# Optimization experiments

Measured on AMD Instinct MI355X. Metric: run time of the kernel, lower is better.

The kernel has to match this reference:

```python
import jax, jax.numpy as jnp
import numpy as np

N_NODES = 50000
IN_DIM = 128
N_EDGES = 500000


def setup_inputs() -> dict:
    key = jax.random.key(0)
    k1, k2, k3, k4 = jax.random.split(key, 4)
    x = jax.random.normal(k1, (N_NODES, IN_DIM), dtype=jnp.float32)
    edge_index = jax.random.randint(k2, (2, N_EDGES), 0, N_NODES, dtype=jnp.int64)
    edge_weight = jax.random.uniform(k3, (N_EDGES,), dtype=jnp.float32)
    # Linear(2*in_dim -> 1): weight flattened to [2*in_dim], scalar bias
    W = jax.random.normal(k4, (2 * IN_DIM,), dtype=jnp.float32) * (1.0 / np.sqrt(2 * IN_DIM))
    b = jnp.zeros((1,), dtype=jnp.float32)
    return {"x": x, "edge_index": edge_index, "edge_weight": edge_weight, "W": W, "b": b}


def reference(x, edge_index, edge_weight, W, b):
    src, dst = edge_index[0], edge_index[1]
    d = x.shape[-1]
    # cat([x[src], x[dst]]) @ W == x[src] @ W[:d] + x[dst] @ W[d:]
    # Pre-project nodes once ([N] each) instead of materializing [E, 2d]
    proj_src = x @ W[:d]          # [N]
    proj_dst = x @ W[d:]          # [N]
    logits = proj_src[src] + proj_dst[dst] + b[0]   # [E]
    prompt_scores = jax.nn.sigmoid(logits)
    return edge_weight * prompt_scores
```

## Files before the change

### kernel.cpp

```cpp
#include <hip/hip_runtime.h>
#include <hip/hip_bf16.h>


#define IN_DIM 128
#define BLOCK 256

__global__ void __launch_bounds__(BLOCK)
edgeprompt_proj(const float* __restrict__ x,
                const float* __restrict__ W,
                float* __restrict__ proj,
                int n_nodes) {
    const int lane = threadIdx.x & 63;
    const int half = lane >> 5;
    const int sl   = lane & 31;
    const int wave = (blockIdx.x * blockDim.x + threadIdx.x) >> 6;

    const float4 ws = *reinterpret_cast<const float4*>(&W[sl * 4]);
    const float4 wd = *reinterpret_cast<const float4*>(&W[IN_DIM + sl * 4]);

    const int n = wave * 2 + half;
    if (n >= n_nodes) return;

    const float4 xv = *reinterpret_cast<const float4*>(&x[(size_t)n * IN_DIM + sl * 4]);
    float ps = xv.x * ws.x + xv.y * ws.y + xv.z * ws.z + xv.w * ws.w;
    float pd = xv.x * wd.x + xv.y * wd.y + xv.z * wd.z + xv.w * wd.w;
    #pragma unroll
    for (int off = 16; off > 0; off >>= 1) {
        ps += __shfl_xor(ps, off);
        pd += __shfl_xor(pd, off);
    }
    if (sl == 0) {
        proj[n] = ps;
        proj[n_nodes + n] = pd;
    }
}

__global__ void __launch_bounds__(BLOCK)
edgeprompt_edges(const int* __restrict__ edge_index,
                 const float* __restrict__ edge_weight,
                 const float* __restrict__ proj,
                 const float* __restrict__ bias_p,
                 float* __restrict__ out,
                 int n_edges, int n_nodes) {
    const int tid = blockIdx.x * blockDim.x + threadIdx.x;
    const float bias = bias_p[0];
    const float* __restrict__ proj_d = proj + n_nodes;

    const int q = tid;
    const int nquads = n_edges >> 2;
    if (q < nquads) {
        const int4   s4 = *reinterpret_cast<const int4*>(&edge_index[q * 4]);
        const int4   d4 = *reinterpret_cast<const int4*>(&edge_index[n_edges + q * 4]);
        const float4 w4 = *reinterpret_cast<const float4*>(&edge_weight[q * 4]);
        float4 o;
        o.x = w4.x / (1.0f + __expf(-(proj[s4.x] + proj_d[d4.x] + bias)));
        o.y = w4.y / (1.0f + __expf(-(proj[s4.y] + proj_d[d4.y] + bias)));
        o.z = w4.z / (1.0f + __expf(-(proj[s4.z] + proj_d[d4.z] + bias)));
        o.w = w4.w / (1.0f + __expf(-(proj[s4.w] + proj_d[d4.w] + bias)));
        *reinterpret_cast<float4*>(&out[q * 4]) = o;
    }
    const int e = (nquads << 2) + tid;
    if (e < n_edges) {
        const int s = edge_index[e];
        const int d = edge_index[n_edges + e];
        out[e] = edge_weight[e] / (1.0f + __expf(-(proj[s] + proj_d[d] + bias)));
    }
}

extern "C" void kernel_launch(void* const* d_in, const int* in_sizes, int n_in,
                              void* d_out, int out_size, void* d_ws, size_t ws_size,
                              hipStream_t stream) {
    const float* x           = (const float*)d_in[0];
    const int*   edge_index  = (const int*)d_in[1];
    const float* edge_weight = (const float*)d_in[2];
    const float* W           = (const float*)d_in[3];
    const float* b           = (const float*)d_in[4];
    float* out = (float*)d_out;

    const int n_nodes = in_sizes[0] / IN_DIM;
    const int n_edges = in_sizes[2];
    float* proj = (float*)d_ws;

    const int blocks1 = (n_nodes + 7) / 8;
    edgeprompt_proj<<<blocks1, BLOCK, 0, stream>>>(x, W, proj, n_nodes);

    const int blocks2 = ((n_edges + 3) / 4 + BLOCK - 1) / BLOCK;
    edgeprompt_edges<<<blocks2, BLOCK, 0, stream>>>(edge_index, edge_weight, proj, b,
                                                    out, n_edges, n_nodes);
}
```

Measured before the change: 17.26 us.

## Grid-stride node projection with 4 nodes per wave; nontemporal edge loads/stores

The projection kernel now assigns four nodes per wave, using 16 lanes per node with two float4 loads each. It runs a grid-stride loop over a capped grid of 2048 blocks instead of launching one block per 8 nodes. The edge kernel switches its streaming index, weight and output accesses to nontemporal loads and stores so they do not pollute cache, keeping the gathered proj array resident. The trade-off is fewer waves in flight for the projection and more per-lane work; nontemporal hints can also slow things if the hardware handles them poorly.

```diff
diff --git a/kernel.cpp b/kernel.cpp
--- a/kernel.cpp
+++ b/kernel.cpp
@@ -4,6 +4,10 @@
 
 #define IN_DIM 128
 #define BLOCK 256
+#define K1_BLOCKS 2048
+
+typedef int   i32x4 __attribute__((ext_vector_type(4)));
+typedef float f32x4 __attribute__((ext_vector_type(4)));
 
 __global__ void __launch_bounds__(BLOCK)
 edgeprompt_proj(const float* __restrict__ x,
@@ -11,27 +15,38 @@
                 float* __restrict__ proj,
                 int n_nodes) {
     const int lane = threadIdx.x & 63;
-    const int half = lane >> 5;
-    const int sl   = lane & 31;
+    const int g    = lane >> 4;
+    const int sg   = lane & 15;
     const int wave = (blockIdx.x * blockDim.x + threadIdx.x) >> 6;
+    const int nwaves = (gridDim.x * blockDim.x) >> 6;
 
-    const float4 ws = *reinterpret_cast<const float4*>(&W[sl * 4]);
-    const float4 wd = *reinterpret_cast<const float4*>(&W[IN_DIM + sl * 4]);
+    const f32x4 ws0 = *reinterpret_cast<const f32x4*>(&W[sg * 4]);
+    const f32x4 ws1 = *reinterpret_cast<const f32x4*>(&W[64 + sg * 4]);
+    const f32x4 wd0 = *reinterpret_cast<const f32x4*>(&W[IN_DIM + sg * 4]);
+    const f32x4 wd1 = *reinterpret_cast<const f32x4*>(&W[IN_DIM + 64 + sg * 4]);
 
-    const int n = wave * 2 + half;
-    if (n >= n_nodes) return;
-
-    const float4 xv = *reinterpret_cast<const float4*>(&x[(size_t)n * IN_DIM + sl * 4]);
-    float ps = xv.x * ws.x + xv.y * ws.y + xv.z * ws.z + xv.w * ws.w;
-    float pd = xv.x * wd.x + xv.y * wd.y + xv.z * wd.z + xv.w * wd.w;
-    #pragma unroll
-    for (int off = 16; off > 0; off >>= 1) {
-        ps += __shfl_xor(ps, off);
-        pd += __shfl_xor(pd, off);
-    }
-    if (sl == 0) {
-        proj[n] = ps;
-        proj[n_nodes + n] = pd;
+    const int nquads = (n_nodes + 3) >> 2;
+    for (int qn = wave; qn < nquads; qn += nwaves) {
+        const int n = qn * 4 + g;
+        float ps = 0.f, pd = 0.f;
+        if (n < n_nodes) {
+            const float* xr = &x[(size_t)n * IN_DIM + sg * 4];
+            const f32x4 x0 = *reinterpret_cast<const f32x4*>(xr);
+            const f32x4 x1 = *reinterpret_cast<const f32x4*>(xr + 64);
+            ps = x0.x * ws0.x + x0.y * ws0.y + x0.z * ws0.z + x0.w * ws0.w
+               + x1.x * ws1.x + x1.y * ws1.y + x1.z * ws1.z + x1.w * ws1.w;
+            pd = x0.x * wd0.x + x0.y * wd0.y + x0.z * wd0.z + x0.w * wd0.w
+               + x1.x * wd1.x + x1.y * wd1.y + x1.z * wd1.z + x1.w * wd1.w;
+        }
+        #pragma unroll
+        for (int off = 8; off > 0; off >>= 1) {
+            ps += __shfl_xor(ps, off);
+            pd += __shfl_xor(pd, off);
+        }
+        if (sg == 0 && n < n_nodes) {
+            proj[n] = ps;
+            proj[n_nodes + n] = pd;
+        }
     }
 }
 
@@ -46,18 +61,20 @@
     const float bias = bias_p[0];
     const float* __restrict__ proj_d = proj + n_nodes;
 
-    const int q = tid;
     const int nquads = n_edges >> 2;
-    if (q < nquads) {
-        const int4   s4 = *reinterpret_cast<const int4*>(&edge_index[q * 4]);
-        const int4   d4 = *reinterpret_cast<const int4*>(&edge_index[n_edges + q * 4]);
-        const float4 w4 = *reinterpret_cast<const float4*>(&edge_weight[q * 4]);
-        float4 o;
+    if (tid < nquads) {
+        const i32x4 s4 = __builtin_nontemporal_load(
+                             reinterpret_cast<const i32x4*>(&edge_index[tid * 4]));
+        const i32x4 d4 = __builtin_nontemporal_load(
+                             reinterpret_cast<const i32x4*>(&edge_index[n_edges + tid * 4]));
+        const f32x4 w4 = __builtin_nontemporal_load(
+                             reinterpret_cast<const f32x4*>(&edge_weight[tid * 4]));
+        f32x4 o;
         o.x = w4.x / (1.0f + __expf(-(proj[s4.x] + proj_d[d4.x] + bias)));
         o.y = w4.y / (1.0f + __expf(-(proj[s4.y] + proj_d[d4.y] + bias)));
         o.z = w4.z / (1.0f + __expf(-(proj[s4.z] + proj_d[d4.z] + bias)));
         o.w = w4.w / (1.0f + __expf(-(proj[s4.w] + proj_d[d4.w] + bias)));
-        *reinterpret_cast<float4*>(&out[q * 4]) = o;
+        __builtin_nontemporal_store(o, reinterpret_cast<f32x4*>(&out[tid * 4]));
     }
     const int e = (nquads << 2) + tid;
     if (e < n_edges) {
@@ -81,7 +98,8 @@
     const int n_edges = in_sizes[2];
     float* proj = (float*)d_ws;
 
-    const int blocks1 = (n_nodes + 7) / 8;
+    const int nquads1 = (n_nodes + 3) / 4;
+    const int blocks1 = min(K1_BLOCKS, (nquads1 + 3) / 4);
     edgeprompt_proj<<<blocks1, BLOCK, 0, stream>>>(x, W, proj, n_nodes);
 
     const int blocks2 = ((n_edges + 3) / 4 + BLOCK - 1) / BLOCK;
```

Measured after the change: 16.71 us. -3.2%, faster.
